# Kernel optimization log

Measured on AMD Instinct MI355X. Metric: run time of the kernel, lower is better.

Reference implementation:

```python
import jax, jax.numpy as jnp
import numpy as np

B, P, K, H, C = 8, 4096, 20, 64, 40  # clouds, points/cloud, knn k, hidden_feat, num_classes
NEG = 0.2  # LeakyReLU negative slope used by the repo MLP


def setup_inputs() -> dict:
    key = jax.random.key(0)
    ks = jax.random.split(key, 16)
    w = lambda k, shape: (jax.random.normal(k, shape, jnp.float32) / np.sqrt(shape[0]))
    return {
        "x": jax.random.normal(ks[0], (B * P, 3), jnp.float32),
        "batch": jnp.repeat(jnp.arange(B, dtype=jnp.int32), P),
        "W1": w(ks[1], (2 * 3, H)), "b1": jnp.zeros((H,), jnp.float32),
        "W2": w(ks[2], (2 * H, H)), "b2": jnp.zeros((H,), jnp.float32),
        "W3": w(ks[3], (2 * H, H)), "b3": jnp.zeros((H,), jnp.float32),
        "Wl": w(ks[4], (3 * H, 1024)), "bl": jnp.zeros((1024,), jnp.float32),
        "Wm1": w(ks[5], (1024, 256)), "bm1": jnp.zeros((256,), jnp.float32),
        "Wm2": w(ks[6], (256, 128)), "bm2": jnp.zeros((128,), jnp.float32),
        "Wo": w(ks[7], (128, C)), "bo": jnp.zeros((C,), jnp.float32),
    }


def _knn_idx(x):
    # x: [B,P,d] -> indices of K nearest neighbors (excluding self): [B,P,K]
    d2 = jnp.sum(x * x, axis=-1)  # [B,P]
    dist = d2[:, :, None] + d2[:, None, :] - 2.0 * jnp.einsum('bpd,bqd->bpq', x, x)
    dist = dist + jnp.eye(x.shape[1], dtype=x.dtype) * 1e10  # mask self-loops
    return jax.lax.top_k(-dist, K)[1]


def _edge_conv(x, W, b):
    # DynamicEdgeConv with max aggregation: nn([x_i, x_j - x_i]) maxed over K neighbors
    idx = _knn_idx(x)                                    # [B,P,K]
    x_j = jax.vmap(lambda xb, ib: xb[ib])(x, idx)        # [B,P,K,d]
    x_i = jnp.broadcast_to(x[:, :, None, :], x_j.shape)  # [B,P,K,d]
    feat = jnp.concatenate([x_i, x_j - x_i], axis=-1)    # [B,P,K,2d]
    h = jax.nn.leaky_relu(feat @ W + b, NEG)             # [B,P,K,H]
    return jnp.max(h, axis=2)                            # [B,P,H]


def reference(x, batch, W1, b1, W2, b2, W3, b3, Wl, bl, Wm1, bm1, Wm2, bm2, Wo, bo):
    # batch is sorted with equal-size clouds -> reshape to [B,P,3]
    xb = x.reshape(B, P, 3)
    x1 = _edge_conv(xb, W1, b1)
    x2 = _edge_conv(x1, W2, b2)
    x3 = _edge_conv(x2, W3, b3)
    h = jnp.concatenate([x1, x2, x3], axis=-1)           # [B,P,3H]
    h = jax.nn.leaky_relu(h @ Wl + bl, NEG)
    h = jax.nn.leaky_relu(h @ Wm1 + bm1, NEG)            # dropout = identity (eval)
    h = jax.nn.leaky_relu(h @ Wm2 + bm2, NEG)
    out = h @ Wo + bo                                    # [B,P,C]
    return jax.nn.log_softmax(out, axis=-1).reshape(B * P, C)
```

## Files before the change

### kernel.cpp

```cpp
#include <hip/hip_runtime.h>
#include <cstddef>
#include <cstdint>

constexpr int B_ = 8, P_ = 4096, K_ = 20, H_ = 64, C_ = 40;
constexpr int NPT = B_ * P_;
#define NEG_SLOPE 0.2f

typedef unsigned long long u64;
typedef unsigned int u32;
typedef unsigned short u16;
typedef __attribute__((ext_vector_type(8))) short bf16x8;
typedef __attribute__((ext_vector_type(4))) float f32x4;

__device__ inline u16 f2bf(float v) {
    u32 bits = __float_as_uint(v);
    return (u16)((bits + 0x7FFFu + ((bits >> 16) & 1)) >> 16);
}
__device__ inline float bf2f(u16 h) { return __uint_as_float((u32)h << 16); }

__device__ __forceinline__ void bubble20f(float (&a)[K_], float key) {
    float carry = key;
#pragma unroll
    for (int s = 0; s < K_; ++s) {
        float as = a[s];
        a[s]  = fminf(carry, as);
        carry = fmaxf(carry, as);
    }
}
__device__ __forceinline__ float mkkey(float dist, int cid) {
    return __uint_as_float((__float_as_uint(dist) & 0xFFFFF000u) | (u32)cid);
}

__global__ __launch_bounds__(256) void d2cvt2_kernel(const float* __restrict__ x,
                                                     float* __restrict__ d2,
                                                     u16* __restrict__ xh,
                                                     u16* __restrict__ xm) {
    int i = blockIdx.x * 256 + threadIdx.x;
    if (i >= NPT) return;
    const float* r = x + (size_t)i * 64;
    float s = 0.f;
#pragma unroll
    for (int d8 = 0; d8 < 64; d8 += 8) {
        float4 v0 = *(const float4*)(r + d8);
        float4 v1 = *(const float4*)(r + d8 + 4);
        s += v0.x * v0.x + v0.y * v0.y + v0.z * v0.z + v0.w * v0.w;
        s += v1.x * v1.x + v1.y * v1.y + v1.z * v1.z + v1.w * v1.w;
        float av[8] = {v0.x, v0.y, v0.z, v0.w, v1.x, v1.y, v1.z, v1.w};
        bf16x8 vh, vm;
#pragma unroll
        for (int j = 0; j < 8; ++j) {
            u16 h = f2bf(av[j]);
            float r1 = av[j] - bf2f(h);
            vh[j] = (short)h; vm[j] = (short)f2bf(r1);
        }
        *(bf16x8*)(xh + (size_t)i * 64 + d8) = vh;
        *(bf16x8*)(xm + (size_t)i * 64 + d8) = vm;
    }
    d2[i] = s;
}

__global__ __launch_bounds__(256) void knnf3_kernel(const float* __restrict__ x,
                                                    int* __restrict__ idx) {
    __shared__ float sC[64][4];

    int b = blockIdx.y;
    int q0 = blockIdx.x * 64;
    const float* xc = x + (size_t)b * P_ * 3;

    int t = threadIdx.x, w = t >> 6, ln = t & 63;
    int q  = ln & 15;
    int ss = ln >> 4;

    int qrow = q0 + w * 16 + q;
    float qx = xc[(size_t)qrow * 3];
    float qy = xc[(size_t)qrow * 3 + 1];
    float qz = xc[(size_t)qrow * 3 + 2];
    float qd2 = qx * qx + qy * qy + qz * qz;

    float a[K_];
#pragma unroll
    for (int s = 0; s < K_; ++s)
        a[s] = __uint_as_float(0x7F7FF000u | (u32)s);
    const float PINV = __uint_as_float(0x7F800000u);
    const float BIGF = __uint_as_float(0x7F7FFFFFu);

    float p0 = PINV, p1 = PINV, p2 = PINV, p3 = PINV;
    int pcnt = 0;
    float kthr = BIGF;

    int scc = t >> 2, scm = t & 3;

#pragma unroll 1
    for (int c0 = 0; c0 < P_; c0 += 64) {
        __syncthreads();
        if (scm < 3) {
            sC[scc][scm] = xc[(size_t)(c0 + scc) * 3 + scm];
        } else {
            float ax = xc[(size_t)(c0 + scc) * 3];
            float ay = xc[(size_t)(c0 + scc) * 3 + 1];
            float az = xc[(size_t)(c0 + scc) * 3 + 2];
            sC[scc][3] = ax * ax + ay * ay + az * az;
        }
        __syncthreads();

#pragma unroll
        for (int nt = 0; nt < 4; ++nt) {
#pragma unroll
            for (int r = 0; r < 4; ++r) {
                int cl = nt * 16 + ss * 4 + r;
                int cID = c0 + cl;
                float4 cv = *(const float4*)&sC[cl][0];
                float dv = (qd2 + cv.w) - 2.f * (qx * cv.x + qy * cv.y + qz * cv.z);
                if (cID == qrow) dv += 1e10f;
                dv = fmaxf(dv, 0.f);
                if (__any(dv <= kthr)) {
                    float key = mkkey(dv, cID);
                    bool pass = key < a[K_ - 1];
                    p3 = pass ? p2 : p3;
                    p2 = pass ? p1 : p2;
                    p1 = pass ? p0 : p1;
                    p0 = pass ? key : p0;
                    pcnt = pass ? pcnt + 1 : pcnt;
                    if (__any(pcnt >= 4)) {
                        bubble20f(a, p3); bubble20f(a, p2); bubble20f(a, p1); bubble20f(a, p0);
                        p0 = p1 = p2 = p3 = PINV; pcnt = 0;
                        kthr = __uint_as_float(__float_as_uint(a[K_ - 1]) | 0xFFFu);
                    }
                }
            }
        }
    }
    bubble20f(a, p3); bubble20f(a, p2); bubble20f(a, p1); bubble20f(a, p0);

    int* op = idx + ((size_t)(b * P_ + qrow)) * K_;
#pragma unroll 1
    for (int k = 0; k < K_; ++k) {
        float v = a[0];
        float v1 = __shfl_xor(v, 16);
        v = fminf(v, v1);
        float v2 = __shfl_xor(v, 32);
        v = fminf(v, v2);
        bool win = (__float_as_uint(a[0]) == __float_as_uint(v));
#pragma unroll
        for (int s = 0; s < K_ - 1; ++s) a[s] = win ? a[s + 1] : a[s];
        a[K_ - 1] = win ? BIGF : a[K_ - 1];
        if (ss == 0)
            op[k] = b * P_ + (int)(__float_as_uint(v) & 0xFFFu);
    }
}

__global__ __launch_bounds__(256) void knnm64_kernel(const u16* __restrict__ xh,
                                                     const u16* __restrict__ xm,
                                                     const float* __restrict__ d2,
                                                     int* __restrict__ idx) {
    __shared__ u16 sH[64 * 64];
    __shared__ u16 sM[64 * 64];
    __shared__ float sd2[P_];

    int b = blockIdx.y;
    int q0 = blockIdx.x * 64;
    const u16* xhb = xh + (size_t)b * P_ * 64;
    const u16* xmb = xm + (size_t)b * P_ * 64;
    const float* d2b = d2 + (size_t)b * P_;

    int t = threadIdx.x, w = t >> 6, ln = t & 63;
    int q  = ln & 15;
    int ss = ln >> 4;

    for (int i = t; i < P_ / 4; i += 256)
        ((float4*)sd2)[i] = ((const float4*)d2b)[i];

    int qrow = q0 + w * 16 + q;
    bf16x8 qh[2], qm[2];
#pragma unroll
    for (int kt = 0; kt < 2; ++kt) {
        size_t off = (size_t)qrow * 64 + kt * 32 + ss * 8;
        qh[kt] = *(const bf16x8*)(xhb + off);
        qm[kt] = *(const bf16x8*)(xmb + off);
    }

    __syncthreads();
    float qd2 = sd2[qrow];

    float a[K_];
#pragma unroll
    for (int s = 0; s < K_; ++s)
        a[s] = __uint_as_float(0x7F7FF000u | (u32)s);
    const float PINV = __uint_as_float(0x7F800000u);
    const float BIGF = __uint_as_float(0x7F7FFFFFu);

    float p0 = PINV, p1 = PINV, p2 = PINV, p3 = PINV;
    int pcnt = 0;
    float kthr = BIGF;

    int sr = t >> 2;
    int sk2 = (t & 3) * 32;
    int sbase = sr * 128, sswz = (sr & 7) << 4;
    size_t sgof = (size_t)sr * 64 + (t & 3) * 16;

#pragma unroll 1
    for (int c0 = 0; c0 < P_; c0 += 64) {
        __syncthreads();
        {
            size_t g = (size_t)c0 * 64 + sgof;
            bf16x8 h0 = *(const bf16x8*)(xhb + g);
            bf16x8 h1 = *(const bf16x8*)(xhb + g + 8);
            bf16x8 m0 = *(const bf16x8*)(xmb + g);
            bf16x8 m1 = *(const bf16x8*)(xmb + g + 8);
            *(bf16x8*)((char*)sH + sbase + (sk2 ^ sswz)) = h0;
            *(bf16x8*)((char*)sH + sbase + ((sk2 + 16) ^ sswz)) = h1;
            *(bf16x8*)((char*)sM + sbase + (sk2 ^ sswz)) = m0;
            *(bf16x8*)((char*)sM + sbase + ((sk2 + 16) ^ sswz)) = m1;
        }
        __syncthreads();

        f32x4 acc[4];
#pragma unroll
        for (int nt = 0; nt < 4; ++nt) {
            acc[nt] = (f32x4){0.f, 0.f, 0.f, 0.f};
            int r = nt * 16 + q;
            int base = r * 128, swz = (r & 7) << 4;
#pragma unroll
            for (int kt = 0; kt < 2; ++kt) {
                int k2 = kt * 64 + ss * 16;
                bf16x8 ch = *(const bf16x8*)((char*)sH + base + (k2 ^ swz));
                bf16x8 cm = *(const bf16x8*)((char*)sM + base + (k2 ^ swz));
                acc[nt] = __builtin_amdgcn_mfma_f32_16x16x32_bf16(cm, qh[kt], acc[nt], 0, 0, 0);
                acc[nt] = __builtin_amdgcn_mfma_f32_16x16x32_bf16(ch, qm[kt], acc[nt], 0, 0, 0);
                acc[nt] = __builtin_amdgcn_mfma_f32_16x16x32_bf16(ch, qh[kt], acc[nt], 0, 0, 0);
            }
        }

        float dvv[4][4];
        float mn = 3.4e38f;
#pragma unroll
        for (int nt = 0; nt < 4; ++nt) {
#pragma unroll
            for (int r = 0; r < 4; ++r) {
                int cID = c0 + nt * 16 + ss * 4 + r;
                float dv = (qd2 + sd2[cID]) - 2.f * acc[nt][r];
                if (cID == qrow) dv += 1e10f;
                dv = fmaxf(dv, 0.f);
                dvv[nt][r] = dv;
                mn = fminf(mn, dv);
            }
        }
        if (__any(mn <= kthr)) {
#pragma unroll
            for (int nt = 0; nt < 4; ++nt) {
#pragma unroll
                for (int r = 0; r < 4; ++r) {
                    float dv = dvv[nt][r];
                    if (__any(dv <= kthr)) {
                        float key = mkkey(dv, c0 + nt * 16 + ss * 4 + r);
                        bool pass = key < a[K_ - 1];
                        p3 = pass ? p2 : p3;
                        p2 = pass ? p1 : p2;
                        p1 = pass ? p0 : p1;
                        p0 = pass ? key : p0;
                        pcnt = pass ? pcnt + 1 : pcnt;
                        if (__any(pcnt >= 4)) {
                            bubble20f(a, p3); bubble20f(a, p2); bubble20f(a, p1); bubble20f(a, p0);
                            p0 = p1 = p2 = p3 = PINV; pcnt = 0;
                            kthr = __uint_as_float(__float_as_uint(a[K_ - 1]) | 0xFFFu);
                        }
                    }
                }
            }
        }
    }
    bubble20f(a, p3); bubble20f(a, p2); bubble20f(a, p1); bubble20f(a, p0);

    int* op = idx + ((size_t)(b * P_ + qrow)) * K_;
#pragma unroll 1
    for (int k = 0; k < K_; ++k) {
        float v = a[0];
        float v1 = __shfl_xor(v, 16);
        v = fminf(v, v1);
        float v2 = __shfl_xor(v, 32);
        v = fminf(v, v2);
        bool win = (__float_as_uint(a[0]) == __float_as_uint(v));
#pragma unroll
        for (int s = 0; s < K_ - 1; ++s) a[s] = win ? a[s + 1] : a[s];
        a[K_ - 1] = win ? BIGF : a[K_ - 1];
        if (ss == 0)
            op[k] = b * P_ + (int)(__float_as_uint(v) & 0xFFFu);
    }
}

__global__ __launch_bounds__(256) void prep_kernel(const float* __restrict__ W2,
                                                   const float* __restrict__ b2,
                                                   const float* __restrict__ W3,
                                                   const float* __restrict__ b3,
                                                   const float* __restrict__ Wl,
                                                   const float* __restrict__ Wm1,
                                                   const float* __restrict__ Wm2,
                                                   float* __restrict__ Wpk2, float* __restrict__ bpk2,
                                                   float* __restrict__ Wpk3, float* __restrict__ bpk3,
                                                   u16* __restrict__ WlT,
                                                   u16* __restrict__ Wm1T,
                                                   u16* __restrict__ Wm2T) {
    int t = blockIdx.x * 256 + threadIdx.x;
    if (t < 8192) {
        int d = t >> 7, h2 = t & 127;
        Wpk2[t] = (h2 < 64) ? W2[d * 64 + h2] : W2[(64 + d) * 64 + (h2 - 64)];
        if (t < 128) bpk2[t] = (t < 64) ? b2[t] : 0.f;
    } else if (t < 16384) {
        int t2 = t - 8192;
        int d = t2 >> 7, h2 = t2 & 127;
        Wpk3[t2] = (h2 < 64) ? W3[d * 64 + h2] : W3[(64 + d) * 64 + (h2 - 64)];
        if (t2 < 128) bpk3[t2] = (t2 < 64) ? b3[t2] : 0.f;
    } else if (t < 212992) {
        int t2 = t - 16384;
        int k = t2 >> 10, n = t2 & 1023;
        WlT[(size_t)n * 192 + k] = f2bf(Wl[t2]);
    } else if (t < 475136) {
        int t2 = t - 212992;
        int k = t2 >> 8, n = t2 & 255;
        Wm1T[(size_t)n * 1024 + k] = f2bf(Wm1[t2]);
    } else if (t < 507904) {
        int t2 = t - 475136;
        int k = t2 >> 7, n = t2 & 127;
        Wm2T[(size_t)n * 256 + k] = f2bf(Wm2[t2]);
    }
}

__global__ __launch_bounds__(256) void uv3_kernel(const float* __restrict__ x,
                                                  const float* __restrict__ W,
                                                  const float* __restrict__ b,
                                                  float* __restrict__ UV) {
    int t = blockIdx.x * 256 + threadIdx.x;
    int p = t >> 7, h2 = t & 127;
    float x0 = x[p * 3], x1 = x[p * 3 + 1], x2 = x[p * 3 + 2];
    float r;
    if (h2 < 64) {
        r = b[h2] + x0 * W[h2] + x1 * W[64 + h2] + x2 * W[128 + h2];
    } else {
        int h = h2 - 64;
        r = x0 * W[192 + h] + x1 * W[256 + h] + x2 * W[320 + h];
    }
    UV[t] = r;
}

__global__ __launch_bounds__(256) void edgemax_kernel(const float* __restrict__ UV,
                                                      const int* __restrict__ idx,
                                                      float* __restrict__ xout) {
    int wv = threadIdx.x >> 6, lane = threadIdx.x & 63;
    int p = blockIdx.x * 4 + wv;
    const float* uvp = UV + (size_t)p * 128;
    float duv = uvp[lane] - uvp[64 + lane];
    const int* ip = idx + (size_t)p * K_;
    int jj[K_];
#pragma unroll
    for (int k = 0; k < K_; ++k) jj[k] = ip[k];
    float m = -3.4e38f;
#pragma unroll
    for (int k = 0; k < K_; ++k) {
        float vj = UV[(size_t)jj[k] * 128 + 64 + lane];
        float t = duv + vj;
        m = fmaxf(m, fmaxf(t, NEG_SLOPE * t));
    }
    xout[(size_t)p * H_ + lane] = m;
}

__global__ __launch_bounds__(256) void gemm_kernel(const float* __restrict__ A1,
                                                   const float* __restrict__ Wm,
                                                   const float* __restrict__ bias,
                                                   float* __restrict__ Cm,
                                                   int M, int N, int Kd, int leaky) {
    __shared__ float sA[32][68];
    __shared__ float sB[32][68];

    int tid = threadIdx.x;
    int row0 = blockIdx.x * 64, col0 = blockIdx.y * 64;
    int tx = tid & 15, ty = tid >> 4;

    int lr  = tid >> 2;
    int lk4 = (tid & 3) * 4;
    int lkb = tid >> 4;
    int lnb = (tid & 15) * 4;

    float acc[4][4] = {};

    for (int k0 = 0; k0 < Kd; k0 += 32) {
        int arow = row0 + lr;
#pragma unroll
        for (int h = 0; h < 32; h += 16) {
            int kk = k0 + lk4 + h;
            const float* src = A1 + (size_t)arow * Kd + kk;
            float4 av = *(const float4*)src;
            sA[lk4 + h + 0][lr] = av.x; sA[lk4 + h + 1][lr] = av.y;
            sA[lk4 + h + 2][lr] = av.z; sA[lk4 + h + 3][lr] = av.w;
        }
        int bcol = col0 + lnb;
#pragma unroll
        for (int h = 0; h < 32; h += 16) {
            float4 bv = make_float4(0.f, 0.f, 0.f, 0.f);
            if (bcol < N) bv = *(const float4*)(Wm + (size_t)(k0 + lkb + h) * N + bcol);
            *(float4*)&sB[lkb + h][lnb] = bv;
        }
        __syncthreads();

#pragma unroll
        for (int kk2 = 0; kk2 < 32; ++kk2) {
            float4 a = *(const float4*)&sA[kk2][ty * 4];
            float4 bb = *(const float4*)&sB[kk2][tx * 4];
            acc[0][0] = fmaf(a.x, bb.x, acc[0][0]); acc[0][1] = fmaf(a.x, bb.y, acc[0][1]);
            acc[0][2] = fmaf(a.x, bb.z, acc[0][2]); acc[0][3] = fmaf(a.x, bb.w, acc[0][3]);
            acc[1][0] = fmaf(a.y, bb.x, acc[1][0]); acc[1][1] = fmaf(a.y, bb.y, acc[1][1]);
            acc[1][2] = fmaf(a.y, bb.z, acc[1][2]); acc[1][3] = fmaf(a.y, bb.w, acc[1][3]);
            acc[2][0] = fmaf(a.z, bb.x, acc[2][0]); acc[2][1] = fmaf(a.z, bb.y, acc[2][1]);
            acc[2][2] = fmaf(a.z, bb.z, acc[2][2]); acc[2][3] = fmaf(a.z, bb.w, acc[2][3]);
            acc[3][0] = fmaf(a.w, bb.x, acc[3][0]); acc[3][1] = fmaf(a.w, bb.y, acc[3][1]);
            acc[3][2] = fmaf(a.w, bb.z, acc[3][2]); acc[3][3] = fmaf(a.w, bb.w, acc[3][3]);
        }
        __syncthreads();
    }

    for (int i = 0; i < 4; ++i) {
        int row = row0 + ty * 4 + i;
        for (int j = 0; j < 4; ++j) {
            int col = col0 + tx * 4 + j;
            if (col < N) {
                float v = acc[i][j] + bias[col];
                if (leaky) v = v > 0.f ? v : NEG_SLOPE * v;
                Cm[(size_t)row * N + col] = v;
            }
        }
    }
}

template <int KD, int OUT_BF16>
__global__ __launch_bounds__(256) void gemm_mfma_kernel(const u16* __restrict__ A,
                                                        const u16* __restrict__ BT,
                                                        const float* __restrict__ bias,
                                                        void* __restrict__ Cout,
                                                        int N, int leaky) {
    __shared__ u16 sA[128 * 64];
    __shared__ u16 sB[128 * 64];

    int t = threadIdx.x;
    int wave = t >> 6, lane = t & 63;
    int wm = wave >> 1, wn = wave & 1;
    int row0 = blockIdx.x * 128;
    int col0 = blockIdx.y * 128;

    f32x4 acc[4][4] = {};

    for (int k0 = 0; k0 < KD; k0 += 64) {
        __syncthreads();
#pragma unroll
        for (int i = 0; i < 4; ++i) {
            int li = t + i * 256;
            int r = li >> 3;
            int kc = (li & 7) * 8;
            bf16x8 v = *(const bf16x8*)(A + (size_t)(row0 + r) * KD + k0 + kc);
            *(bf16x8*)((char*)sA + r * 128 + ((kc * 2) ^ ((r & 7) << 4))) = v;
        }
#pragma unroll
        for (int i = 0; i < 4; ++i) {
            int li = t + i * 256;
            int n = li >> 3;
            int kc = (li & 7) * 8;
            bf16x8 v = *(const bf16x8*)(BT + (size_t)(col0 + n) * KD + k0 + kc);
            *(bf16x8*)((char*)sB + n * 128 + ((kc * 2) ^ ((n & 7) << 4))) = v;
        }
        __syncthreads();

#pragma unroll
        for (int kk = 0; kk < 2; ++kk) {
            int kb = kk * 64 + (lane >> 4) * 16;
            bf16x8 af[4], bfr[4];
#pragma unroll
            for (int mi = 0; mi < 4; ++mi) {
                int r = wm * 64 + mi * 16 + (lane & 15);
                af[mi] = *(const bf16x8*)((char*)sA + r * 128 + (kb ^ ((r & 7) << 4)));
            }
#pragma unroll
            for (int ni = 0; ni < 4; ++ni) {
                int n = wn * 64 + ni * 16 + (lane & 15);
                bfr[ni] = *(const bf16x8*)((char*)sB + n * 128 + (kb ^ ((n & 7) << 4)));
            }
#pragma unroll
            for (int mi = 0; mi < 4; ++mi)
#pragma unroll
                for (int ni = 0; ni < 4; ++ni)
                    acc[mi][ni] = __builtin_amdgcn_mfma_f32_16x16x32_bf16(
                        af[mi], bfr[ni], acc[mi][ni], 0, 0, 0);
        }
    }

#pragma unroll
    for (int ni = 0; ni < 4; ++ni) {
        int col = col0 + wn * 64 + ni * 16 + (lane & 15);
        float bs = bias[col];
#pragma unroll
        for (int mi = 0; mi < 4; ++mi) {
#pragma unroll
            for (int r = 0; r < 4; ++r) {
                int row = row0 + wm * 64 + mi * 16 + (lane >> 4) * 4 + r;
                float v = acc[mi][ni][r] + bs;
                if (leaky) v = v > 0.f ? v : NEG_SLOPE * v;
                if (OUT_BF16)
                    ((u16*)Cout)[(size_t)row * N + col] = f2bf(v);
                else
                    ((float*)Cout)[(size_t)row * N + col] = v;
            }
        }
    }
}

__global__ __launch_bounds__(256) void gemm_mfma_cat_kernel(const float* __restrict__ x1,
                                                            const float* __restrict__ x2,
                                                            const float* __restrict__ x3,
                                                            const u16* __restrict__ BT,
                                                            const float* __restrict__ bias,
                                                            u16* __restrict__ Cout,
                                                            int N) {
    __shared__ u16 sA[128 * 64];
    __shared__ u16 sB[128 * 64];

    int t = threadIdx.x;
    int wave = t >> 6, lane = t & 63;
    int wm = wave >> 1, wn = wave & 1;
    int row0 = blockIdx.x * 128;
    int col0 = blockIdx.y * 128;

    f32x4 acc[4][4] = {};

#pragma unroll 1
    for (int k0 = 0; k0 < 192; k0 += 64) {
        const float* src = (k0 == 0) ? x1 : (k0 == 64) ? x2 : x3;
        __syncthreads();
#pragma unroll
        for (int i = 0; i < 4; ++i) {
            int li = t + i * 256;
            int r = li >> 3;
            int kc = (li & 7) * 8;
            const float* sp = src + (size_t)(row0 + r) * 64 + kc;
            float4 a0 = *(const float4*)sp;
            float4 a1 = *(const float4*)(sp + 4);
            bf16x8 v;
            v[0] = (short)f2bf(a0.x); v[1] = (short)f2bf(a0.y);
            v[2] = (short)f2bf(a0.z); v[3] = (short)f2bf(a0.w);
            v[4] = (short)f2bf(a1.x); v[5] = (short)f2bf(a1.y);
            v[6] = (short)f2bf(a1.z); v[7] = (short)f2bf(a1.w);
            *(bf16x8*)((char*)sA + r * 128 + ((kc * 2) ^ ((r & 7) << 4))) = v;
        }
#pragma unroll
        for (int i = 0; i < 4; ++i) {
            int li = t + i * 256;
            int n = li >> 3;
            int kc = (li & 7) * 8;
            bf16x8 v = *(const bf16x8*)(BT + (size_t)(col0 + n) * 192 + k0 + kc);
            *(bf16x8*)((char*)sB + n * 128 + ((kc * 2) ^ ((n & 7) << 4))) = v;
        }
        __syncthreads();

#pragma unroll
        for (int kk = 0; kk < 2; ++kk) {
            int kb = kk * 64 + (lane >> 4) * 16;
            bf16x8 af[4], bfr[4];
#pragma unroll
            for (int mi = 0; mi < 4; ++mi) {
                int r = wm * 64 + mi * 16 + (lane & 15);
                af[mi] = *(const bf16x8*)((char*)sA + r * 128 + (kb ^ ((r & 7) << 4)));
            }
#pragma unroll
            for (int ni = 0; ni < 4; ++ni) {
                int n = wn * 64 + ni * 16 + (lane & 15);
                bfr[ni] = *(const bf16x8*)((char*)sB + n * 128 + (kb ^ ((n & 7) << 4)));
            }
#pragma unroll
            for (int mi = 0; mi < 4; ++mi)
#pragma unroll
                for (int ni = 0; ni < 4; ++ni)
                    acc[mi][ni] = __builtin_amdgcn_mfma_f32_16x16x32_bf16(
                        af[mi], bfr[ni], acc[mi][ni], 0, 0, 0);
        }
    }

#pragma unroll
    for (int ni = 0; ni < 4; ++ni) {
        int col = col0 + wn * 64 + ni * 16 + (lane & 15);
        float bs = bias[col];
#pragma unroll
        for (int mi = 0; mi < 4; ++mi) {
#pragma unroll
            for (int r = 0; r < 4; ++r) {
                int row = row0 + wm * 64 + mi * 16 + (lane >> 4) * 4 + r;
                float v = acc[mi][ni][r] + bs;
                v = v > 0.f ? v : NEG_SLOPE * v;
                Cout[(size_t)row * N + col] = f2bf(v);
            }
        }
    }
}

__global__ __launch_bounds__(256) void lsm_wo_kernel(const float* __restrict__ act3,
                                                     const float* __restrict__ Wo,
                                                     const float* __restrict__ bo,
                                                     float* __restrict__ out) {
    __shared__ float sWo[128 * 44];
    __shared__ float sAct[4][128];

    int t = threadIdx.x;
    for (int i = t; i < 128 * 40; i += 256) {
        int k = i / 40, c = i % 40;
        sWo[k * 44 + c] = Wo[i];
    }
    __syncthreads();

    int wv = t >> 6, lane = t & 63;
    int row = blockIdx.x * 4 + wv;
    sAct[wv][lane]      = act3[(size_t)row * 128 + lane];
    sAct[wv][64 + lane] = act3[(size_t)row * 128 + 64 + lane];

    float acc = (lane < C_) ? bo[lane] : -3.4e38f;
    if (lane < C_) {
#pragma unroll 8
        for (int k = 0; k < 128; ++k)
            acc = fmaf(sAct[wv][k], sWo[k * 44 + lane], acc);
    }
    float m = acc;
#pragma unroll
    for (int s = 1; s < 64; s <<= 1) m = fmaxf(m, __shfl_xor(m, s));
    float e = (lane < C_) ? expf(acc - m) : 0.f;
    float sum = e;
#pragma unroll
    for (int s = 1; s < 64; s <<= 1) sum += __shfl_xor(sum, s);
    if (lane < C_) out[(size_t)row * C_ + lane] = acc - m - logf(sum);
}

extern "C" void kernel_launch(void* const* d_in, const int* in_sizes, int n_in,
                              void* d_out, int out_size, void* d_ws, size_t ws_size,
                              hipStream_t stream) {
    const float* x   = (const float*)d_in[0];
    const float* W1  = (const float*)d_in[2];
    const float* b1  = (const float*)d_in[3];
    const float* W2  = (const float*)d_in[4];
    const float* b2  = (const float*)d_in[5];
    const float* W3  = (const float*)d_in[6];
    const float* b3  = (const float*)d_in[7];
    const float* Wl  = (const float*)d_in[8];
    const float* bl  = (const float*)d_in[9];
    const float* Wm1 = (const float*)d_in[10];
    const float* bm1 = (const float*)d_in[11];
    const float* Wm2 = (const float*)d_in[12];
    const float* bm2 = (const float*)d_in[13];
    const float* Wo  = (const float*)d_in[14];
    const float* bo  = (const float*)d_in[15];
    float* out = (float*)d_out;

    char* ws = (char*)d_ws;
    float* x1   = (float*)(ws);
    float* x2   = (float*)(ws + 8388608);
    float* x3   = (float*)(ws + 16777216);
    int*   idx  = (int*)  (ws + 25165824);
    float* d2   = (float*)(ws + 27787264);
    char* hb = ws + 27918336;
    u16*   xhs  = (u16*)(hb);
    u16*   xms  = (u16*)(hb + 4194304);
    float* UV   = (float*)(hb);
    float* Wpk2 = (float*)(ws + 44695552);
    float* bpk2 = (float*)(ws + 44728320);
    float* Wpk3 = (float*)(ws + 44728832);
    float* bpk3 = (float*)(ws + 44761600);
    u16*   WlT  = (u16*)  (ws + 44762112);
    u16*   Wm1T = (u16*)  (ws + 45155328);
    u16*   Wm2T = (u16*)  (ws + 45679616);
    u16*   act1 = (u16*)(hb);
    u16*   act2 = (u16*)(ws + 45745152);
    float* act3 = (float*)(hb);

    prep_kernel<<<1984, 256, 0, stream>>>(W2, b2, W3, b3, Wl, Wm1, Wm2,
                                          Wpk2, bpk2, Wpk3, bpk3, WlT, Wm1T, Wm2T);

    knnf3_kernel<<<dim3(P_ / 64, B_), 256, 0, stream>>>(x, idx);
    uv3_kernel<<<NPT * 128 / 256, 256, 0, stream>>>(x, W1, b1, UV);
    edgemax_kernel<<<NPT / 4, 256, 0, stream>>>(UV, idx, x1);
    d2cvt2_kernel<<<NPT / 256, 256, 0, stream>>>(x1, d2, xhs, xms);
    knnm64_kernel<<<dim3(P_ / 64, B_), 256, 0, stream>>>(xhs, xms, d2, idx);
    gemm_kernel<<<dim3(NPT / 64, 2), 256, 0, stream>>>(x1, Wpk2, bpk2, UV, NPT, 128, 64, 0);
    edgemax_kernel<<<NPT / 4, 256, 0, stream>>>(UV, idx, x2);
    d2cvt2_kernel<<<NPT / 256, 256, 0, stream>>>(x2, d2, xhs, xms);
    knnm64_kernel<<<dim3(P_ / 64, B_), 256, 0, stream>>>(xhs, xms, d2, idx);
    gemm_kernel<<<dim3(NPT / 64, 2), 256, 0, stream>>>(x2, Wpk3, bpk3, UV, NPT, 128, 64, 0);
    edgemax_kernel<<<NPT / 4, 256, 0, stream>>>(UV, idx, x3);

    for (int c = 0; c < 4; ++c) {
        size_t r0 = (size_t)c * 8192;
        gemm_mfma_cat_kernel<<<dim3(64, 8), 256, 0, stream>>>(x1 + r0 * 64, x2 + r0 * 64,
                                                              x3 + r0 * 64, WlT, bl, act1, 1024);
        gemm_mfma_kernel<1024, 1><<<dim3(64, 2), 256, 0, stream>>>(act1, Wm1T, bm1, act2, 256, 1);
        gemm_mfma_kernel<256, 0><<<dim3(64, 1), 256, 0, stream>>>(act2, Wm2T, bm2, act3, 128, 1);
        lsm_wo_kernel<<<2048, 256, 0, stream>>>(act3, Wo, bo, out + r0 * C_);
    }
}
```

Before: 895.3 us.

## Pre-pack xyz+norm for first kNN and double candidate tile in MFMA kNN

Adds a pack kernel that stores each point as float4 (x,y,z,|x|^2), so the first kNN kernel reads candidates straight from global/L2 with vector loads and no longer stages them through shared memory, which removes both barriers per tile. The 64-dim kNN kernel now stages 128 candidates per iteration instead of 64, halving the number of barrier/load phases and doubling MFMA work per sync. In exchange it uses more LDS (32KB of tiles plus 16KB of squared norms), keeps more accumulator registers live (acc[8], dvv[8][4]), which can lower occupancy, and adds one extra kernel launch.

```diff
diff --git a/kernel.cpp b/kernel.cpp
--- a/kernel.cpp
+++ b/kernel.cpp
@@ -29,6 +29,14 @@
 }
 __device__ __forceinline__ float mkkey(float dist, int cid) {
     return __uint_as_float((__float_as_uint(dist) & 0xFFFFF000u) | (u32)cid);
+}
+
+__global__ __launch_bounds__(256) void pack4_kernel(const float* __restrict__ x,
+                                                    float4* __restrict__ xp) {
+    int i = blockIdx.x * 256 + threadIdx.x;
+    if (i >= NPT) return;
+    float ax = x[(size_t)i * 3], ay = x[(size_t)i * 3 + 1], az = x[(size_t)i * 3 + 2];
+    xp[i] = make_float4(ax, ay, az, ax * ax + ay * ay + az * az);
 }
 
 __global__ __launch_bounds__(256) void d2cvt2_kernel(const float* __restrict__ x,
@@ -59,23 +67,18 @@
     d2[i] = s;
 }
 
-__global__ __launch_bounds__(256) void knnf3_kernel(const float* __restrict__ x,
+__global__ __launch_bounds__(256) void knnf3_kernel(const float4* __restrict__ xp,
                                                     int* __restrict__ idx) {
-    __shared__ float sC[64][4];
-
     int b = blockIdx.y;
     int q0 = blockIdx.x * 64;
-    const float* xc = x + (size_t)b * P_ * 3;
+    const float4* xb = xp + (size_t)b * P_;
 
     int t = threadIdx.x, w = t >> 6, ln = t & 63;
     int q  = ln & 15;
     int ss = ln >> 4;
 
     int qrow = q0 + w * 16 + q;
-    float qx = xc[(size_t)qrow * 3];
-    float qy = xc[(size_t)qrow * 3 + 1];
-    float qz = xc[(size_t)qrow * 3 + 2];
-    float qd2 = qx * qx + qy * qy + qz * qz;
+    float4 qv = xb[qrow];
 
     float a[K_];
 #pragma unroll
@@ -88,29 +91,19 @@
     int pcnt = 0;
     float kthr = BIGF;
 
-    int scc = t >> 2, scm = t & 3;
-
 #pragma unroll 1
     for (int c0 = 0; c0 < P_; c0 += 64) {
-        __syncthreads();
-        if (scm < 3) {
-            sC[scc][scm] = xc[(size_t)(c0 + scc) * 3 + scm];
-        } else {
-            float ax = xc[(size_t)(c0 + scc) * 3];
-            float ay = xc[(size_t)(c0 + scc) * 3 + 1];
-            float az = xc[(size_t)(c0 + scc) * 3 + 2];
-            sC[scc][3] = ax * ax + ay * ay + az * az;
-        }
-        __syncthreads();
-
 #pragma unroll
         for (int nt = 0; nt < 4; ++nt) {
+            float4 cv[4];
+#pragma unroll
+            for (int r = 0; r < 4; ++r)
+                cv[r] = xb[c0 + nt * 16 + ss * 4 + r];
 #pragma unroll
             for (int r = 0; r < 4; ++r) {
-                int cl = nt * 16 + ss * 4 + r;
-                int cID = c0 + cl;
-                float4 cv = *(const float4*)&sC[cl][0];
-                float dv = (qd2 + cv.w) - 2.f * (qx * cv.x + qy * cv.y + qz * cv.z);
+                int cID = c0 + nt * 16 + ss * 4 + r;
+                float dv = (qv.w + cv[r].w)
+                         - 2.f * (qv.x * cv[r].x + qv.y * cv[r].y + qv.z * cv[r].z);
                 if (cID == qrow) dv += 1e10f;
                 dv = fmaxf(dv, 0.f);
                 if (__any(dv <= kthr)) {
@@ -153,8 +146,8 @@
                                                      const u16* __restrict__ xm,
                                                      const float* __restrict__ d2,
                                                      int* __restrict__ idx) {
-    __shared__ u16 sH[64 * 64];
-    __shared__ u16 sM[64 * 64];
+    __shared__ u16 sH[128 * 64];
+    __shared__ u16 sM[128 * 64];
     __shared__ float sd2[P_];
 
     int b = blockIdx.y;
@@ -193,30 +186,31 @@
     int pcnt = 0;
     float kthr = BIGF;
 
-    int sr = t >> 2;
-    int sk2 = (t & 3) * 32;
+    int sr = t >> 1;
+    int half = t & 1;
     int sbase = sr * 128, sswz = (sr & 7) << 4;
-    size_t sgof = (size_t)sr * 64 + (t & 3) * 16;
+    size_t sgof = (size_t)sr * 64 + half * 32;
+    int kb0 = half * 64;
 
 #pragma unroll 1
-    for (int c0 = 0; c0 < P_; c0 += 64) {
+    for (int c0 = 0; c0 < P_; c0 += 128) {
         __syncthreads();
         {
             size_t g = (size_t)c0 * 64 + sgof;
-            bf16x8 h0 = *(const bf16x8*)(xhb + g);
-            bf16x8 h1 = *(const bf16x8*)(xhb + g + 8);
-            bf16x8 m0 = *(const bf16x8*)(xmb + g);
-            bf16x8 m1 = *(const bf16x8*)(xmb + g + 8);
-            *(bf16x8*)((char*)sH + sbase + (sk2 ^ sswz)) = h0;
-            *(bf16x8*)((char*)sH + sbase + ((sk2 + 16) ^ sswz)) = h1;
-            *(bf16x8*)((char*)sM + sbase + (sk2 ^ sswz)) = m0;
-            *(bf16x8*)((char*)sM + sbase + ((sk2 + 16) ^ sswz)) = m1;
-        }
-        __syncthreads();
-
-        f32x4 acc[4];
-#pragma unroll
-        for (int nt = 0; nt < 4; ++nt) {
+#pragma unroll
+            for (int e = 0; e < 4; ++e) {
+                bf16x8 hv = *(const bf16x8*)(xhb + g + e * 8);
+                bf16x8 mv = *(const bf16x8*)(xmb + g + e * 8);
+                int k2 = kb0 + e * 16;
+                *(bf16x8*)((char*)sH + sbase + (k2 ^ sswz)) = hv;
+                *(bf16x8*)((char*)sM + sbase + (k2 ^ sswz)) = mv;
+            }
+        }
+        __syncthreads();
+
+        f32x4 acc[8];
+#pragma unroll
+        for (int nt = 0; nt < 8; ++nt) {
             acc[nt] = (f32x4){0.f, 0.f, 0.f, 0.f};
             int r = nt * 16 + q;
             int base = r * 128, swz = (r & 7) << 4;
@@ -231,10 +225,10 @@
             }
         }
 
-        float dvv[4][4];
+        float dvv[8][4];
         float mn = 3.4e38f;
 #pragma unroll
-        for (int nt = 0; nt < 4; ++nt) {
+        for (int nt = 0; nt < 8; ++nt) {
 #pragma unroll
             for (int r = 0; r < 4; ++r) {
                 int cID = c0 + nt * 16 + ss * 4 + r;
@@ -247,7 +241,7 @@
         }
         if (__any(mn <= kthr)) {
 #pragma unroll
-            for (int nt = 0; nt < 4; ++nt) {
+            for (int nt = 0; nt < 8; ++nt) {
 #pragma unroll
                 for (int r = 0; r < 4; ++r) {
                     float dv = dvv[nt][r];
@@ -659,6 +653,7 @@
     int*   idx  = (int*)  (ws + 25165824);
     float* d2   = (float*)(ws + 27787264);
     char* hb = ws + 27918336;
+    float4* xp  = (float4*)(hb);
     u16*   xhs  = (u16*)(hb);
     u16*   xms  = (u16*)(hb + 4194304);
     float* UV   = (float*)(hb);
@@ -676,7 +671,8 @@
     prep_kernel<<<1984, 256, 0, stream>>>(W2, b2, W3, b3, Wl, Wm1, Wm2,
                                           Wpk2, bpk2, Wpk3, bpk3, WlT, Wm1T, Wm2T);
 
-    knnf3_kernel<<<dim3(P_ / 64, B_), 256, 0, stream>>>(x, idx);
+    pack4_kernel<<<NPT / 256, 256, 0, stream>>>(x, xp);
+    knnf3_kernel<<<dim3(P_ / 64, B_), 256, 0, stream>>>(xp, idx);
     uv3_kernel<<<NPT * 128 / 256, 256, 0, stream>>>(x, W1, b1, UV);
     edgemax_kernel<<<NPT / 4, 256, 0, stream>>>(UV, idx, x1);
     d2cvt2_kernel<<<NPT / 256, 256, 0, stream>>>(x1, d2, xhs, xms);
```

Result: no change. 889.1 us (-0.7%).
